# Kernel optimization log

Measured on AMD Instinct MI355X. Metric: run time of the kernel, lower is better.

Reference implementation:

```python
import jax, jax.numpy as jnp
import numpy as np

L, D, H, R = 8, 1024, 16, 16
HD = D // H  # head dim


def setup_inputs() -> dict:
    key = jax.random.key(0)
    ks = jax.random.split(key, 7)
    s = 0.02  # init scale for stability
    return {
        "x": jax.random.normal(ks[0], (2, 1024, D), jnp.float32),
        "Wqkv": jax.random.normal(ks[1], (L, D, 3 * D), jnp.float32) * s,
        "Aqkv": jax.random.normal(ks[2], (L, D, R), jnp.float32) * s,
        "Bqkv": jax.random.normal(ks[3], (L, R, 3 * D), jnp.float32) * s,
        "Wproj": jax.random.normal(ks[4], (L, D, D), jnp.float32) * s,
        "Aproj": jax.random.normal(ks[5], (L, D, R), jnp.float32) * s,
        "Bproj": jax.random.normal(ks[6], (L, R, D), jnp.float32) * s,
    }


def _forward(x, Wqkv, Aqkv, Bqkv, Wproj, Aproj, Bproj):
    B, S, _ = x.shape
    # causal mask [S, S]
    mask = jnp.tril(jnp.ones((S, S), bool))

    def layer(h, p):
        Wq, Aq, Bq, Wp, Ap, Bp = p
        # LoRA merge exactly as the module: p + A @ B, then dense matmul
        Wq_m = Wq + Aq @ Bq            # [D, 3D]
        Wp_m = Wp + Ap @ Bp            # [D, D]
        qkv = h @ Wq_m                 # [B, S, 3D]
        q, k, v = jnp.split(qkv, 3, axis=-1)
        q = q.reshape(B, S, H, HD).transpose(0, 2, 1, 3)  # [B,H,S,hd]
        k = k.reshape(B, S, H, HD).transpose(0, 2, 1, 3)
        v = v.reshape(B, S, H, HD).transpose(0, 2, 1, 3)
        scores = jnp.einsum("bhqd,bhkd->bhqk", q, k) / np.sqrt(HD)
        scores = jnp.where(mask, scores, jnp.finfo(scores.dtype).min)
        attn = jax.nn.softmax(scores, axis=-1)
        o = jnp.einsum("bhqk,bhkd->bhqd", attn, v)        # [B,H,S,hd]
        o = o.transpose(0, 2, 1, 3).reshape(B, S, D)
        return h + o @ Wp_m, None

    out, _ = jax.lax.scan(layer, x, (Wqkv, Aqkv, Bqkv, Wproj, Aproj, Bproj))
    return out


def reference(x, Wqkv, Aqkv, Bqkv, Wproj, Aproj, Bproj):
    return _forward(x, Wqkv, Aqkv, Bqkv, Wproj, Aproj, Bproj)
```

## Files before the change

kernel.cpp:

```cpp
#include <hip/hip_runtime.h>
#include <hip/hip_bf16.h>


typedef unsigned short ushort_t;
typedef __attribute__((ext_vector_type(8))) short bf16x8;
typedef __attribute__((ext_vector_type(4))) float f32x4;

__device__ __forceinline__ unsigned short f2bf(float f) {
    union { float f; unsigned int u; } x; x.f = f;
    unsigned int r = x.u + 0x7fffu + ((x.u >> 16) & 1u);
    return (unsigned short)(r >> 16);
}

__device__ __forceinline__ f32x4 mfma16(bf16x8 a, bf16x8 b, f32x4 c) {
    return __builtin_amdgcn_mfma_f32_16x16x32_bf16(a, b, c, 0, 0, 0);
}

typedef const __attribute__((address_space(1))) unsigned int* gas_ptr;
typedef __attribute__((address_space(3))) unsigned int* las_ptr;
__device__ __forceinline__ void lds_stage16(const void* g, void* l) {
    __builtin_amdgcn_global_load_lds((gas_ptr)(unsigned long long)g,
                                     (las_ptr)(unsigned int)(unsigned long long)l,
                                     16, 0, 0);
}

#define RORMAX(x, C)                                                           \
    x = fmaxf(x, __int_as_float(__builtin_amdgcn_mov_dpp(                      \
                     __float_as_int(x), C, 0xf, 0xf, false)));
#define RORADD(x, C)                                                           \
    x += __int_as_float(__builtin_amdgcn_mov_dpp(                              \
        __float_as_int(x), C, 0xf, 0xf, false));

__global__ __launch_bounds__(256) void convert_x(
    const float4* __restrict__ in, float4* __restrict__ outF,
    ushort4* __restrict__ outB, int n4) {
    int i = blockIdx.x * 256 + threadIdx.x;
    if (i < n4) {
        float4 v = in[i];
        outF[i] = v;
        ushort4 o;
        o.x = f2bf(v.x); o.y = f2bf(v.y); o.z = f2bf(v.z); o.w = f2bf(v.w);
        outB[i] = o;
    }
}

__global__ __launch_bounds__(256) void merge_T2(
    const float* __restrict__ Wq, const float* __restrict__ Aq,
    const float* __restrict__ Bq, unsigned short* __restrict__ WTq,
    const float* __restrict__ Wp, const float* __restrict__ Ap,
    const float* __restrict__ Bp, unsigned short* __restrict__ WTp) {
    __shared__ float Asl[32][17];
    __shared__ __align__(16) float tW[32 * 128];
    int bid = blockIdx.x;
    const float *W, *A, *Bm;
    unsigned short* WT;
    int N, bx, by, bz;
    if (bid < 6144) {
        N = 3072; bx = bid % 24; int u = bid / 24; by = u & 31; bz = u >> 5;
        W = Wq; A = Aq; Bm = Bq; WT = WTq;
    } else {
        bid -= 6144;
        N = 1024; bx = bid & 7; int u = bid >> 3; by = u & 31; bz = u >> 5;
        W = Wp; A = Ap; Bm = Bp; WT = WTp;
    }
    W  += (size_t)bz * 1024 * N;
    A  += (size_t)bz * 1024 * 16;
    Bm += (size_t)bz * 16 * N;
    WT += (size_t)bz * N * 1024;
    const int j0 = bx * 128, i0 = by * 32;
    const int tid = threadIdx.x;
    const int w = tid >> 6, lane = tid & 63;

    #pragma unroll
    for (int s = 0; s < 4; s++) {
        int w4s = w * 4 + s;
        int tr = w4s * 2 + (lane >> 5);
        lds_stage16(W + (size_t)(i0 + tr) * N + j0 + (lane & 31) * 4,
                    (char*)tW + w4s * 1024);
    }
    if (tid < 128) {
        int r = tid >> 2, c4 = (tid & 3) * 4;
        float4 a = *(const float4*)&A[(size_t)(i0 + r) * 16 + c4];
        Asl[r][c4 + 0] = a.x; Asl[r][c4 + 1] = a.y;
        Asl[r][c4 + 2] = a.z; Asl[r][c4 + 3] = a.w;
    }
    const int jj = tid >> 1, half = tid & 1;
    float bcol[16];
    #pragma unroll
    for (int r = 0; r < 16; r++)
        bcol[r] = Bm[(size_t)r * N + j0 + jj];
    __builtin_amdgcn_sched_barrier(0);
    __syncthreads();

    bf16x8 o0, o1;
    #pragma unroll
    for (int c = 0; c < 16; c++) {
        int rloc = half * 16 + c;
        float v = tW[rloc * 128 + jj];
        #pragma unroll
        for (int r = 0; r < 16; r++)
            v += Asl[rloc][r] * bcol[r];
        unsigned short b = f2bf(v);
        if (c < 8) o0[c] = (short)b; else o1[c - 8] = (short)b;
    }
    unsigned short* dst = &WT[(size_t)(j0 + jj) * 1024 + i0 + half * 16];
    *(bf16x8*)dst = o0;
    *(bf16x8*)(dst + 8) = o1;
}

__global__ __launch_bounds__(256) void gemm_bf16_128(
    const unsigned short* __restrict__ A,
    const unsigned short* __restrict__ BT,
    unsigned short* __restrict__ outB,
    unsigned short* __restrict__ VT,
    int M, int N, int K) {
    __shared__ __align__(16) unsigned short As[2][128 * 32];
    __shared__ __align__(16) unsigned short Bs[2][128 * 32];
    const int tid = threadIdx.x;
    const int m0 = blockIdx.y * 128, n0 = blockIdx.x * 128;
    const int w = tid >> 6, lane = tid & 63;
    const int wm = (w >> 1) * 64, wn = (w & 1) * 64;
    const int lr = lane & 15, quad = lane >> 4;
    const int srow = w * 16 + (lane >> 2);
    const int skof = (lane & 3) * 8;

    f32x4 acc[4][4] = {};

    for (int k0 = 0; k0 < K; k0 += 64) {
        __syncthreads();
        #pragma unroll
        for (int h = 0; h < 2; h++) {
            lds_stage16(A  + (size_t)(m0 + srow)      * K + k0 + h * 32 + skof,
                        (char*)As[h] + w * 1024);
            lds_stage16(A  + (size_t)(m0 + 64 + srow) * K + k0 + h * 32 + skof,
                        (char*)As[h] + 4096 + w * 1024);
            lds_stage16(BT + (size_t)(n0 + srow)      * K + k0 + h * 32 + skof,
                        (char*)Bs[h] + w * 1024);
            lds_stage16(BT + (size_t)(n0 + 64 + srow) * K + k0 + h * 32 + skof,
                        (char*)Bs[h] + 4096 + w * 1024);
        }
        __syncthreads();

        #pragma unroll
        for (int h = 0; h < 2; h++) {
            bf16x8 af[4], bfr[4];
            #pragma unroll
            for (int i = 0; i < 4; i++) {
                af[i]  = *(const bf16x8*)&As[h][(wm + i * 16 + lr) * 32 + quad * 8];
                bfr[i] = *(const bf16x8*)&Bs[h][(wn + i * 16 + lr) * 32 + quad * 8];
            }
            #pragma unroll
            for (int i = 0; i < 4; i++)
                #pragma unroll
                for (int j = 0; j < 4; j++)
                    acc[i][j] = mfma16(af[i], bfr[j], acc[i][j]);
        }
    }
    if (n0 < 2048) {
        #pragma unroll
        for (int i = 0; i < 4; i++)
            #pragma unroll
            for (int j = 0; j < 4; j++)
                #pragma unroll
                for (int r = 0; r < 4; r++) {
                    int row = m0 + wm + i * 16 + quad * 4 + r;
                    int col = n0 + wn + j * 16 + lr;
                    float v = acc[i][j][r];
                    if (col < 1024) v *= 0.125f * 1.44269504f;
                    outB[(size_t)row * N + col] = f2bf(v);
                }
    } else {
        const int b = m0 >> 10;
        #pragma unroll
        for (int i = 0; i < 4; i++) {
            int row0 = m0 + wm + i * 16 + quad * 4;
            int s = row0 & 1023;
            #pragma unroll
            for (int j = 0; j < 4; j++) {
                int hd = n0 - 2048 + wn + j * 16 + lr;
                ushort4 o;
                o.x = f2bf(acc[i][j][0]); o.y = f2bf(acc[i][j][1]);
                o.z = f2bf(acc[i][j][2]); o.w = f2bf(acc[i][j][3]);
                *(ushort4*)&VT[((size_t)b * 1024 + hd) * 1024 + s] = o;
            }
        }
    }
}

__global__ __launch_bounds__(256) void gemm_bf16_64(
    const unsigned short* __restrict__ A,
    const unsigned short* __restrict__ BT,
    const float* __restrict__ res,
    float* __restrict__ outF,
    unsigned short* __restrict__ outB,
    int M, int N, int K) {
    __shared__ __align__(16) unsigned short As[2][2][64 * 32];
    __shared__ __align__(16) unsigned short Bs[2][2][64 * 32];
    const int tid = threadIdx.x;
    const int m0 = blockIdx.y * 64, n0 = blockIdx.x * 64;
    const int w = tid >> 6, lane = tid & 63;
    const int wm = (w >> 1) * 32, wn = (w & 1) * 32;
    const int lr = lane & 15, quad = lane >> 4;
    const int srow = w * 16 + (lane >> 2);
    const int skof = (lane & 3) * 8;

    f32x4 acc[2][2] = {};

    auto stage = [&](int k0, int buf) {
        #pragma unroll
        for (int h = 0; h < 2; h++) {
            lds_stage16(A  + (size_t)(m0 + srow) * K + k0 + h * 32 + skof,
                        (char*)As[buf][h] + w * 1024);
            lds_stage16(BT + (size_t)(n0 + srow) * K + k0 + h * 32 + skof,
                        (char*)Bs[buf][h] + w * 1024);
        }
    };

    const int nk = K >> 6;
    stage(0, 0);
    for (int t = 0; t < nk; t++) {
        __syncthreads();
        if (t + 1 < nk) stage((t + 1) << 6, (t + 1) & 1);
        const int cur = t & 1;
        #pragma unroll
        for (int h = 0; h < 2; h++) {
            bf16x8 af[2], bfr[2];
            #pragma unroll
            for (int i = 0; i < 2; i++) {
                af[i]  = *(const bf16x8*)&As[cur][h][(wm + i * 16 + lr) * 32 + quad * 8];
                bfr[i] = *(const bf16x8*)&Bs[cur][h][(wn + i * 16 + lr) * 32 + quad * 8];
            }
            #pragma unroll
            for (int i = 0; i < 2; i++)
                #pragma unroll
                for (int j = 0; j < 2; j++)
                    acc[i][j] = mfma16(af[i], bfr[j], acc[i][j]);
        }
    }
    #pragma unroll
    for (int i = 0; i < 2; i++)
        #pragma unroll
        for (int j = 0; j < 2; j++)
            #pragma unroll
            for (int r = 0; r < 4; r++) {
                int row = m0 + wm + i * 16 + quad * 4 + r;
                int col = n0 + wn + j * 16 + lr;
                float v = acc[i][j][r] + res[(size_t)row * N + col];
                if (outF) outF[(size_t)row * N + col] = v;
                if (outB) outB[(size_t)row * N + col] = f2bf(v);
            }
}

__global__ __launch_bounds__(256) void attn_kernel(
    const unsigned short* __restrict__ qkv,
    const unsigned short* __restrict__ VT,
    unsigned short* __restrict__ O) {
    __shared__ __align__(16) unsigned short Ks[2][2][64 * 32];
    __shared__ __align__(16) unsigned short Vs[2][2][64 * 32];
    __shared__ __align__(16) unsigned short pl[4][16 * 72];
    const int tid = threadIdx.x;
    const int w = tid >> 6, lane = tid & 63;
    const int lr = lane & 15, quad = lane >> 4;
    const int bh = blockIdx.y, b = bh >> 4, h = bh & 15;
    const int qblk = (bh < 16) ? blockIdx.x : (15 - blockIdx.x);
    const int qb = qblk * 64 + w * 16;
    const int srow = w * 16 + (lane >> 2);
    const int skof = (lane & 3) * 8;

    const size_t rowQ = (size_t)(b * 1024 + qb + lr) * 3072 + h * 64;
    bf16x8 aq0 = *(const bf16x8*)&qkv[rowQ + quad * 8];
    bf16x8 aq1 = *(const bf16x8*)&qkv[rowQ + 32 + quad * 8];

    float m_i[4], l_i[4];
    f32x4 oacc[4] = {};
    #pragma unroll
    for (int r = 0; r < 4; r++) { m_i[r] = -1e30f; l_i[r] = 0.f; }

    auto stage = [&](int kt64, int buf) {
        const int kt = kt64 << 6;
        const size_t gK = (size_t)(b * 1024 + kt + srow) * 3072 + 1024 + h * 64;
        lds_stage16(qkv + gK + skof,      (char*)Ks[buf][0] + w * 1024);
        lds_stage16(qkv + gK + 32 + skof, (char*)Ks[buf][1] + w * 1024);
        const size_t gV = ((size_t)bh * 64 + srow) * 1024 + kt;
        lds_stage16(VT + gV + skof,       (char*)Vs[buf][0] + w * 1024);
        lds_stage16(VT + gV + 32 + skof,  (char*)Vs[buf][1] + w * 1024);
    };

    const int nkt = qblk + 1;
    stage(0, 0);
    for (int kt64 = 0; kt64 < nkt; kt64++) {
        __syncthreads();
        if (kt64 + 1 < nkt) stage(kt64 + 1, (kt64 + 1) & 1);
        const int cur = kt64 & 1;
        const int kt = kt64 << 6;

        f32x4 s[4] = {};
        #pragma unroll
        for (int nh = 0; nh < 4; nh++) {
            bf16x8 kb0 = *(const bf16x8*)&Ks[cur][0][(nh * 16 + lr) * 32 + quad * 8];
            bf16x8 kb1 = *(const bf16x8*)&Ks[cur][1][(nh * 16 + lr) * 32 + quad * 8];
            s[nh] = mfma16(aq0, kb0, s[nh]);
            s[nh] = mfma16(aq1, kb1, s[nh]);
        }
        float mx[4];
        if (kt + 64 > qb) {
            #pragma unroll
            for (int r = 0; r < 4; r++) {
                int qrow = qb + quad * 4 + r;
                #pragma unroll
                for (int nh = 0; nh < 4; nh++) {
                    int kcol = kt + nh * 16 + lr;
                    s[nh][r] = (kcol <= qrow) ? s[nh][r] : -1e30f;
                }
            }
        }
        #pragma unroll
        for (int r = 0; r < 4; r++) {
            mx[r] = fmaxf(fmaxf(s[0][r], s[1][r]), fmaxf(s[2][r], s[3][r]));
            RORMAX(mx[r], 0x121) RORMAX(mx[r], 0x122)
            RORMAX(mx[r], 0x124) RORMAX(mx[r], 0x128)
        }
        float al[4];
        #pragma unroll
        for (int r = 0; r < 4; r++) {
            float mnew = fmaxf(m_i[r], mx[r]);
            al[r] = exp2f(m_i[r] - mnew);
            m_i[r] = mnew;
            float lsum = 0.f;
            #pragma unroll
            for (int nh = 0; nh < 4; nh++) {
                float p = exp2f(s[nh][r] - mnew);
                s[nh][r] = p;
                lsum += p;
            }
            l_i[r] = l_i[r] * al[r] + lsum;
        }
        #pragma unroll
        for (int dt = 0; dt < 4; dt++)
            #pragma unroll
            for (int r = 0; r < 4; r++) oacc[dt][r] *= al[r];
        #pragma unroll
        for (int nh = 0; nh < 4; nh++)
            #pragma unroll
            for (int r = 0; r < 4; r++)
                pl[w][(quad * 4 + r) * 72 + nh * 16 + lr] = f2bf(s[nh][r]);
        bf16x8 ap0 = *(const bf16x8*)&pl[w][lr * 72 + quad * 8];
        bf16x8 ap1 = *(const bf16x8*)&pl[w][lr * 72 + 32 + quad * 8];
        #pragma unroll
        for (int dt = 0; dt < 4; dt++) {
            bf16x8 vb0 = *(const bf16x8*)&Vs[cur][0][(dt * 16 + lr) * 32 + quad * 8];
            bf16x8 vb1 = *(const bf16x8*)&Vs[cur][1][(dt * 16 + lr) * 32 + quad * 8];
            oacc[dt] = mfma16(ap0, vb0, oacc[dt]);
            oacc[dt] = mfma16(ap1, vb1, oacc[dt]);
        }
    }
    #pragma unroll
    for (int r = 0; r < 4; r++) {
        RORADD(l_i[r], 0x121) RORADD(l_i[r], 0x122)
        RORADD(l_i[r], 0x124) RORADD(l_i[r], 0x128)
    }
    #pragma unroll
    for (int dt = 0; dt < 4; dt++)
        #pragma unroll
        for (int r = 0; r < 4; r++) {
            int row = b * 1024 + qb + quad * 4 + r;
            int col = h * 64 + dt * 16 + lr;
            O[(size_t)row * 1024 + col] = f2bf(oacc[dt][r] / l_i[r]);
        }
}

extern "C" void kernel_launch(void* const* d_in, const int* in_sizes, int n_in,
                              void* d_out, int out_size, void* d_ws, size_t ws_size,
                              hipStream_t stream) {
    const float* x     = (const float*)d_in[0];
    const float* Wqkv  = (const float*)d_in[1];
    const float* Aqkv  = (const float*)d_in[2];
    const float* Bqkv  = (const float*)d_in[3];
    const float* Wproj = (const float*)d_in[4];
    const float* Aproj = (const float*)d_in[5];
    const float* Bproj = (const float*)d_in[6];
    float* out = (float*)d_out;

    char* ws = (char*)d_ws;
    float* h_f32 = (float*)ws;                    ws += (size_t)2048 * 1024 * 4;
    unsigned short* h_bf   = (unsigned short*)ws; ws += (size_t)2048 * 1024 * 2;
    unsigned short* qkv_bf = (unsigned short*)ws; ws += (size_t)2048 * 3072 * 2;
    unsigned short* VT     = (unsigned short*)ws; ws += (size_t)32 * 64 * 1024 * 2;
    unsigned short* O_bf   = (unsigned short*)ws; ws += (size_t)2048 * 1024 * 2;
    unsigned short* WqT8   = (unsigned short*)ws; ws += (size_t)8 * 3072 * 1024 * 2;
    unsigned short* WpT8   = (unsigned short*)ws; ws += (size_t)8 * 1024 * 1024 * 2;

    convert_x<<<2048, 256, 0, stream>>>((const float4*)x, (float4*)h_f32,
                                        (ushort4*)h_bf, 2048 * 1024 / 4);
    merge_T2<<<8192, 256, 0, stream>>>(Wqkv, Aqkv, Bqkv, WqT8,
                                       Wproj, Aproj, Bproj, WpT8);

    for (int l = 0; l < 8; l++) {
        const unsigned short* WqT = WqT8 + (size_t)l * 3072 * 1024;
        const unsigned short* WpT = WpT8 + (size_t)l * 1024 * 1024;
        gemm_bf16_128<<<dim3(24, 16), 256, 0, stream>>>(h_bf, WqT, qkv_bf, VT,
                                                        2048, 3072, 1024);
        attn_kernel<<<dim3(16, 32), 256, 0, stream>>>(qkv_bf, VT, O_bf);
        float* outF = (l == 7) ? out : h_f32;
        gemm_bf16_64<<<dim3(16, 32), 256, 0, stream>>>(O_bf, WpT, h_f32, outF,
                                                       h_bf, 2048, 1024, 1024);
    }
}
```

Before: 710.0 us.

## Halve QKV GEMM M-tile and double-buffer LDS staging across K iterations

The QKV projection GEMM now uses 64x128 tiles instead of 128x128, doubling the grid from 384 to 768 blocks so the 256 CUs get better occupancy and load balance. It also double-buffers the LDS tiles, issuing the async global-to-LDS loads for the next K step before computing on the current one. This hides load latency behind the MFMA work and removes one barrier per iteration. The cost is less data reuse per tile and more total global traffic for the weight matrix.

```diff
diff --git a/kernel.cpp b/kernel.cpp
--- a/kernel.cpp
+++ b/kernel.cpp
@@ -108,49 +108,55 @@
     *(bf16x8*)(dst + 8) = o1;
 }
 
-__global__ __launch_bounds__(256) void gemm_bf16_128(
+__global__ __launch_bounds__(256) void gemm_qkv(
     const unsigned short* __restrict__ A,
     const unsigned short* __restrict__ BT,
     unsigned short* __restrict__ outB,
     unsigned short* __restrict__ VT,
     int M, int N, int K) {
-    __shared__ __align__(16) unsigned short As[2][128 * 32];
-    __shared__ __align__(16) unsigned short Bs[2][128 * 32];
+    __shared__ __align__(16) unsigned short As[2][2][64 * 32];
+    __shared__ __align__(16) unsigned short Bs[2][2][128 * 32];
     const int tid = threadIdx.x;
-    const int m0 = blockIdx.y * 128, n0 = blockIdx.x * 128;
+    const int m0 = blockIdx.y * 64, n0 = blockIdx.x * 128;
     const int w = tid >> 6, lane = tid & 63;
-    const int wm = (w >> 1) * 64, wn = (w & 1) * 64;
+    const int wm = (w >> 1) * 32, wn = (w & 1) * 64;
     const int lr = lane & 15, quad = lane >> 4;
-    const int srow = w * 16 + (lane >> 2);
+    const int srowA = w * 16 + (lane >> 2);
     const int skof = (lane & 3) * 8;
 
-    f32x4 acc[4][4] = {};
-
-    for (int k0 = 0; k0 < K; k0 += 64) {
+    f32x4 acc[2][4] = {};
+
+    auto stage = [&](int k0, int buf) {
+        #pragma unroll
+        for (int h = 0; h < 2; h++) {
+            lds_stage16(A + (size_t)(m0 + srowA) * K + k0 + h * 32 + skof,
+                        (char*)As[buf][h] + w * 1024);
+            #pragma unroll
+            for (int s = 0; s < 2; s++) {
+                int srowB = w * 32 + s * 16 + (lane >> 2);
+                lds_stage16(BT + (size_t)(n0 + srowB) * K + k0 + h * 32 + skof,
+                            (char*)Bs[buf][h] + (w * 2 + s) * 1024);
+            }
+        }
+    };
+
+    const int nk = K >> 6;
+    stage(0, 0);
+    for (int t = 0; t < nk; t++) {
         __syncthreads();
+        if (t + 1 < nk) stage((t + 1) << 6, (t + 1) & 1);
+        const int cur = t & 1;
         #pragma unroll
         for (int h = 0; h < 2; h++) {
-            lds_stage16(A  + (size_t)(m0 + srow)      * K + k0 + h * 32 + skof,
-                        (char*)As[h] + w * 1024);
-            lds_stage16(A  + (size_t)(m0 + 64 + srow) * K + k0 + h * 32 + skof,
-                        (char*)As[h] + 4096 + w * 1024);
-            lds_stage16(BT + (size_t)(n0 + srow)      * K + k0 + h * 32 + skof,
-                        (char*)Bs[h] + w * 1024);
-            lds_stage16(BT + (size_t)(n0 + 64 + srow) * K + k0 + h * 32 + skof,
-                        (char*)Bs[h] + 4096 + w * 1024);
-        }
-        __syncthreads();
-
-        #pragma unroll
-        for (int h = 0; h < 2; h++) {
-            bf16x8 af[4], bfr[4];
-            #pragma unroll
-            for (int i = 0; i < 4; i++) {
-                af[i]  = *(const bf16x8*)&As[h][(wm + i * 16 + lr) * 32 + quad * 8];
-                bfr[i] = *(const bf16x8*)&Bs[h][(wn + i * 16 + lr) * 32 + quad * 8];
-            }
-            #pragma unroll
-            for (int i = 0; i < 4; i++)
+            bf16x8 af[2], bfr[4];
+            #pragma unroll
+            for (int i = 0; i < 2; i++)
+                af[i] = *(const bf16x8*)&As[cur][h][(wm + i * 16 + lr) * 32 + quad * 8];
+            #pragma unroll
+            for (int j = 0; j < 4; j++)
+                bfr[j] = *(const bf16x8*)&Bs[cur][h][(wn + j * 16 + lr) * 32 + quad * 8];
+            #pragma unroll
+            for (int i = 0; i < 2; i++)
                 #pragma unroll
                 for (int j = 0; j < 4; j++)
                     acc[i][j] = mfma16(af[i], bfr[j], acc[i][j]);
@@ -158,7 +164,7 @@
     }
     if (n0 < 2048) {
         #pragma unroll
-        for (int i = 0; i < 4; i++)
+        for (int i = 0; i < 2; i++)
             #pragma unroll
             for (int j = 0; j < 4; j++)
                 #pragma unroll
@@ -172,7 +178,7 @@
     } else {
         const int b = m0 >> 10;
         #pragma unroll
-        for (int i = 0; i < 4; i++) {
+        for (int i = 0; i < 2; i++) {
             int row0 = m0 + wm + i * 16 + quad * 4;
             int s = row0 & 1023;
             #pragma unroll
@@ -398,8 +404,8 @@
     for (int l = 0; l < 8; l++) {
         const unsigned short* WqT = WqT8 + (size_t)l * 3072 * 1024;
         const unsigned short* WpT = WpT8 + (size_t)l * 1024 * 1024;
-        gemm_bf16_128<<<dim3(24, 16), 256, 0, stream>>>(h_bf, WqT, qkv_bf, VT,
-                                                        2048, 3072, 1024);
+        gemm_qkv<<<dim3(24, 32), 256, 0, stream>>>(h_bf, WqT, qkv_bf, VT,
+                                                   2048, 3072, 1024);
         attn_kernel<<<dim3(16, 32), 256, 0, stream>>>(qkv_bf, VT, O_bf);
         float* outF = (l == 7) ? out : h_f32;
         gemm_bf16_64<<<dim3(16, 32), 256, 0, stream>>>(O_bf, WpT, h_f32, outF,
```

Result: faster. 682.5 us (-3.9%).
